# Optimization experiments

Measured on AMD Instinct MI355X. Metric: run time of the kernel, lower is better.

Reference implementation:

```python
import jax, jax.numpy as jnp
import numpy as np

N_BASIS = 8
CUTOFF = 5.0
NORM_FACTOR = 16.0


def setup_inputs() -> dict:
    key = jax.random.key(0)
    ks = jax.random.split(key, 10)
    N, E, C = 20000, 320000, 32
    s = 1.0 / np.sqrt(C)
    return {
        "node0": jax.random.normal(ks[0], (N, C), jnp.float32),
        "node1": jax.random.normal(ks[1], (N, C, 3), jnp.float32),
        "node2": jax.random.normal(ks[2], (N, C, 3, 3), jnp.float32),
        "rij": jax.random.normal(ks[3], (E, 3), jnp.float32) * 1.5,
        "Wrad": jax.random.normal(ks[4], (11, N_BASIS, C), jnp.float32) * 0.3,
        "U": jax.random.normal(ks[5], (3, C, C), jnp.float32) * s,
        "V": jax.random.normal(ks[6], (8, C, C), jnp.float32) * s,
        "Wg": jax.random.normal(ks[7], (3, C, C), jnp.float32) * s,
        "idx_i": jax.random.randint(ks[8], (E,), 0, N),
        "idx_j": jax.random.randint(ks[9], (E,), 0, N),
    }


def reference(node0, node1, node2, rij, Wrad, U, V, Wg, idx_i, idx_j):
    N, C = node0.shape
    # radial basis (Gaussian RBF * cosine cutoff envelope)
    dist = jnp.sqrt(jnp.sum(rij * rij, -1) + 1e-12)           # [E]
    rhat = rij / dist[:, None]                                 # [E,3]
    centers = jnp.linspace(0.5, CUTOFF, N_BASIS, dtype=node0.dtype)
    fc = 0.5 * (jnp.cos(jnp.pi * jnp.clip(dist / CUTOFF, 0.0, 1.0)) + 1.0)
    rbf = jnp.exp(-4.0 * (dist[:, None] - centers) ** 2) * fc[:, None]  # [E,B]
    # per-coupling-path radial filters: 11 paths (in_way, r_way, out_way)
    w = jnp.einsum('eb,pbc->pec', rbf, Wrad)                   # [11,E,C]
    # gather neighbor (node_j) features per edge
    g0 = node0[idx_j]                                          # [E,C]
    g1 = node1[idx_j]                                          # [E,C,3]
    g2 = node2[idx_j]                                          # [E,C,3,3]
    m1 = rhat                                                  # [E,3]
    m2 = rhat[:, :, None] * rhat[:, None, :]                   # [E,3,3]
    # graph conv: contract node_j tensor with r-way moment, weighted by radial filter
    # paths: 0:(0,0,0) 1:(0,1,1) 2:(0,2,2) 3:(1,0,1) 4:(1,1,0) 5:(1,1,2)
    #        6:(1,2,1) 7:(2,0,2) 8:(2,1,1) 9:(2,2,0) 10:(2,2,2)
    msg0 = (g0 * w[0]
            + jnp.einsum('eca,ea->ec', g1, m1) * w[4]
            + jnp.einsum('ecab,eab->ec', g2, m2) * w[9])
    msg1 = (jnp.einsum('ec,ea->eca', g0 * w[1], m1)
            + g1 * w[3][:, :, None]
            + jnp.einsum('eca,eab->ecb', g1, m2) * w[6][:, :, None]
            + jnp.einsum('ecab,eb->eca', g2, m1) * w[8][:, :, None])
    msg2 = (jnp.einsum('ec,eab->ecab', g0 * w[2], m2)
            + jnp.einsum('eca,eb->ecab', g1 * w[5][:, :, None], m1)
            + g2 * w[7][:, :, None, None]
            + jnp.einsum('ecab,ebd->ecad', g2, m2) * w[10][:, :, None, None])
    # scatter_add aggregation into per-atom features, normalized
    a0 = jax.ops.segment_sum(msg0, idx_i, num_segments=N) / NORM_FACTOR
    a1 = jax.ops.segment_sum(msg1, idx_i, num_segments=N) / NORM_FACTOR
    a2 = jax.ops.segment_sum(msg2, idx_i, num_segments=N) / NORM_FACTOR
    # multi-body self-interaction (2-body linear U + 3-body products V)
    y0 = (jnp.einsum('nc,cd->nd', a0, U[0])
          + jnp.einsum('nc,cd->nd', a0 * a0, V[0])
          + jnp.einsum('nc,cd->nd', jnp.einsum('nca,nca->nc', a1, a1), V[3])
          + jnp.einsum('nc,cd->nd', jnp.einsum('ncab,ncab->nc', a2, a2), V[6]))
    y1 = (jnp.einsum('nca,cd->nda', a1, U[1])
          + jnp.einsum('nca,cd->nda', a0[:, :, None] * a1, V[1])
          + jnp.einsum('nca,cd->nda', jnp.einsum('nca,ncab->ncb', a1, a2), V[5]))
    y2 = (jnp.einsum('ncab,cd->ndab', a2, U[2])
          + jnp.einsum('ncab,cd->ndab', a0[:, :, None, None] * a2, V[2])
          + jnp.einsum('ncab,cd->ndab', a1[:, :, :, None] * a1[:, :, None, :], V[4])
          + jnp.einsum('ncab,cd->ndab', jnp.einsum('ncab,ncbd->ncad', a2, a2), V[7]))
    # gated nonlinearity (scalar channel gates tensor ways) + residual add
    new0 = node0 + jax.nn.silu(y0 @ Wg[0])
    new1 = node1 + y1 * jax.nn.silu(y0 @ Wg[1])[:, :, None]
    new2 = node2 + y2 * jax.nn.silu(y0 @ Wg[2])[:, :, None, None]
    return (new0, new1, new2)
```

## Files before the change

kernel.cpp:

```cpp
#include <hip/hip_runtime.h>
#include <hip/hip_fp16.h>

#define NCH 32
#define NB 8
#define NPB 8

typedef __attribute__((ext_vector_type(2))) _Float16 half2r;

__device__ __forceinline__ unsigned short f2h(float f) {
    return __half_as_ushort(__float2half_rn(f));
}
__device__ __forceinline__ float h2f_lo(unsigned int u) {
    half2r v = __builtin_bit_cast(half2r, u);
    return (float)v.x;
}
__device__ __forceinline__ float h2f_hi(unsigned int u) {
    half2r v = __builtin_bit_cast(half2r, u);
    return (float)v.y;
}
__device__ __forceinline__ unsigned int pack2h(float lo, float hi) {
    return (unsigned int)f2h(lo) | ((unsigned int)f2h(hi) << 16);
}

__device__ __forceinline__ float fdot2u(unsigned int a, unsigned int b, float c) {
#if __has_builtin(__builtin_amdgcn_fdot2)
    return __builtin_amdgcn_fdot2(__builtin_bit_cast(half2r, a),
                                  __builtin_bit_cast(half2r, b), c, false);
#else
    half2r av = __builtin_bit_cast(half2r, a);
    half2r bv = __builtin_bit_cast(half2r, b);
    return c + (float)av.x * (float)bv.x + (float)av.y * (float)bv.y;
#endif
}

__device__ __forceinline__ void acc8h(float& y, uint4 w, uint4 f) {
    y = fdot2u(w.x, f.x, y);
    y = fdot2u(w.y, f.y, y);
    y = fdot2u(w.z, f.z, y);
    y = fdot2u(w.w, f.w, y);
}
__device__ __forceinline__ void acc8fh(float& y, uint4 w, float4 a, float4 b) {
    y += h2f_lo(w.x) * a.x + h2f_hi(w.x) * a.y + h2f_lo(w.y) * a.z + h2f_hi(w.y) * a.w
       + h2f_lo(w.z) * b.x + h2f_hi(w.z) * b.y + h2f_lo(w.w) * b.z + h2f_hi(w.w) * b.w;
}

__global__ __launch_bounds__(256) void prep_kernel(
    const float* __restrict__ node0, const float* __restrict__ node1,
    const float* __restrict__ node2,
    const float* __restrict__ U, const float* __restrict__ V,
    const float* __restrict__ Wg, const float* __restrict__ Wrad,
    uint2* __restrict__ t0g, uint4* __restrict__ t1g,
    unsigned short* __restrict__ t2g,
    unsigned short* __restrict__ wswz, unsigned int* __restrict__ wradp,
    int N, int TB)
{
    __shared__ float s1[8 * 96];
    __shared__ float s2[8 * 288];
    const int bx = blockIdx.x;

    if (bx < TB) {
        const int nb0 = bx * 8;
        const int remN = N - nb0;
        if (remN >= 8) {
            const float4* src1 = reinterpret_cast<const float4*>(node1 + (size_t)nb0 * 96);
            float4* d1 = reinterpret_cast<float4*>(s1);
            for (int i = threadIdx.x; i < 192; i += 256) d1[i] = src1[i];
            const float4* src2 = reinterpret_cast<const float4*>(node2 + (size_t)nb0 * 288);
            float4* d2 = reinterpret_cast<float4*>(s2);
            for (int i = threadIdx.x; i < 576; i += 256) d2[i] = src2[i];
        } else {
            const int tot1 = remN * 96;
            for (int i = threadIdx.x; i < 768; i += 256)
                s1[i] = (i < tot1) ? node1[(size_t)nb0 * 96 + i] : 0.f;
            const int tot2 = remN * 288;
            for (int i = threadIdx.x; i < 2304; i += 256)
                s2[i] = (i < tot2) ? node2[(size_t)nb0 * 288 + i] : 0.f;
        }
        __syncthreads();

        const int g = threadIdx.x >> 5;
        const int c = threadIdx.x & 31;
        const int n = nb0 + g;
        if (n >= N) return;

        float G0 = node0[(size_t)n * 32 + c];
        float G1[3];
        #pragma unroll
        for (int a = 0; a < 3; ++a) G1[a] = s1[g * 96 + c * 3 + a];
        float G2[9];
        #pragma unroll
        for (int k = 0; k < 9; ++k) G2[k] = s2[g * 288 + c * 9 + k];

        const size_t b = ((size_t)n << 5) + c;
        uint2 P0;
        P0.x = pack2h(G0, G1[0]);
        P0.y = pack2h(G1[1], G1[2]);
        uint4 P1;
        P1.x = pack2h(G2[0], G2[1]);
        P1.y = pack2h(G2[2], G2[3]);
        P1.z = pack2h(G2[4], G2[5]);
        P1.w = pack2h(G2[6], G2[7]);
        t0g[b] = P0;
        t1g[b] = P1;
        t2g[b] = f2h(G2[8]);
        return;
    }

    const int r = bx - TB;
    if (r < 56) {
        int idx = r * 256 + threadIdx.x;
        if (idx >= 14 * 1024) return;
        int m = idx >> 10, rr = idx & 1023;
        int c = rr >> 5, d = rr & 31;
        float v;
        if (m < 3)       v = U[m * 1024 + c * 32 + d];
        else if (m < 11) v = V[(m - 3) * 1024 + c * 32 + d];
        else             v = Wg[(m - 11) * 1024 + c * 32 + d];
        wswz[m * 1024 + (c >> 3) * 256 + d * 8 + (c & 7)] = f2h(v);
        return;
    }

    {
        int idx = (r - 56) * 256 + threadIdx.x;
        if (idx >= 11 * 4 * 32) return;
        int c = idx & 31, bb = (idx >> 5) & 3, p = idx >> 7;
        float lo = Wrad[p * 256 + (2 * bb) * 32 + c] * (1.0f / 16.0f);
        float hi = Wrad[p * 256 + (2 * bb + 1) * 32 + c] * (1.0f / 16.0f);
        wradp[c * 44 + p * 4 + bb] = pack2h(lo, hi);
    }
}

__global__ __launch_bounds__(256) void hist_kernel(
    const int* __restrict__ idx_i, int* __restrict__ counts, int E)
{
    int e = blockIdx.x * 256 + threadIdx.x;
    if (e < E) atomicAdd(&counts[idx_i[e]], 1);
}

__global__ __launch_bounds__(256) void scan_reduce_kernel(
    const int* __restrict__ counts, int* __restrict__ blocksums, int N)
{
    const int tid = threadIdx.x;
    const int base = blockIdx.x * 1024;
    int v = 0;
    #pragma unroll
    for (int k = 0; k < 4; ++k) {
        int i = base + tid * 4 + k;
        if (i < N) v += counts[i];
    }
    #pragma unroll
    for (int off = 1; off < 64; off <<= 1) v += __shfl_xor(v, off, 64);
    __shared__ int wsum[4];
    if ((tid & 63) == 0) wsum[tid >> 6] = v;
    __syncthreads();
    if (tid == 0) blocksums[blockIdx.x] = wsum[0] + wsum[1] + wsum[2] + wsum[3];
}

__global__ void scan_top_kernel(
    const int* __restrict__ blocksums, int* __restrict__ bases,
    int* __restrict__ offsets, int nb, int N)
{
    int l = threadIdx.x;
    int v = (l < nb) ? blocksums[l] : 0;
    int incl = v;
    #pragma unroll
    for (int off = 1; off < 64; off <<= 1) {
        int t = __shfl_up(incl, off, 64);
        if (l >= off) incl += t;
    }
    if (l < nb) bases[l] = incl - v;
    if (l == nb - 1) offsets[N] = incl;
}

__global__ __launch_bounds__(256) void scan_write_kernel(
    int* __restrict__ cursor, const int* __restrict__ bases,
    int* __restrict__ offsets, int N)
{
    const int tid = threadIdx.x;
    const int i0 = blockIdx.x * 1024 + tid * 4;
    int v[4]; int lsum = 0;
    #pragma unroll
    for (int k = 0; k < 4; ++k) {
        int i = i0 + k;
        v[k] = (i < N) ? cursor[i] : 0;
        lsum += v[k];
    }
    int incl = lsum;
    #pragma unroll
    for (int off = 1; off < 64; off <<= 1) {
        int t = __shfl_up(incl, off, 64);
        if ((tid & 63) >= off) incl += t;
    }
    __shared__ int wsum[4];
    if ((tid & 63) == 63) wsum[tid >> 6] = incl;
    __syncthreads();
    int add = bases[blockIdx.x];
    for (int w = 0; w < (tid >> 6); ++w) add += wsum[w];
    int run = add + incl - lsum;
    #pragma unroll
    for (int k = 0; k < 4; ++k) {
        int i = i0 + k;
        if (i < N) { offsets[i] = run; cursor[i] = run; run += v[k]; }
    }
}

__global__ __launch_bounds__(256) void scatter_meta_kernel(
    const int* __restrict__ idx_i, const int* __restrict__ idx_j,
    const float* __restrict__ rij, int* __restrict__ cursor,
    int* __restrict__ jord, float4* __restrict__ meta2, int E)
{
    int e = blockIdx.x * 256 + threadIdx.x;
    if (e >= E) return;
    float rx = rij[3 * e + 0], ry = rij[3 * e + 1], rz = rij[3 * e + 2];
    float sq = rx * rx + ry * ry + rz * rz + 1e-12f;
    float inv = rsqrtf(sq);
    float dist = sq * inv;
    float tcl = fminf(dist * 0.2f, 1.0f);
    float fc = 0.5f * (__cosf(3.14159265358979f * tcl) + 1.0f);
    float rbf[NB];
    #pragma unroll
    for (int b = 0; b < NB; ++b) {
        float dd = dist - (0.5f + (float)b * (4.5f / 7.0f));
        rbf[b] = __expf(-4.0f * dd * dd) * fc;
    }
    unsigned int rb01 = pack2h(rbf[0], rbf[1]);
    unsigned int rb23 = pack2h(rbf[2], rbf[3]);
    unsigned int rb45 = pack2h(rbf[4], rbf[5]);
    unsigned int rb67 = pack2h(rbf[6], rbf[7]);
    int slot = atomicAdd(&cursor[idx_i[e]], 1);
    jord[slot] = idx_j[e];
    meta2[2 * slot + 0] = make_float4(rx * inv, ry * inv, rz * inv, __uint_as_float(rb01));
    meta2[2 * slot + 1] = make_float4(__uint_as_float(rb23), __uint_as_float(rb45),
                                      __uint_as_float(rb67), 0.0f);
}

__device__ __forceinline__ void edge_compute(
    uint2 P0, uint4 P1, unsigned short g28, float4 M0, float4 M1,
    const uint4 wrq[11], float& A0, float (&A1)[3], float (&A2)[9])
{
    const float h0 = M0.x, h1 = M0.y, h2 = M0.z;
    const unsigned int rb01 = __float_as_uint(M0.w);
    const unsigned int rb23 = __float_as_uint(M1.x);
    const unsigned int rb45 = __float_as_uint(M1.y);
    const unsigned int rb67 = __float_as_uint(M1.z);

    float w[11];
    #pragma unroll
    for (int p = 0; p < 11; ++p)
        w[p] = fdot2u(rb01, wrq[p].x,
               fdot2u(rb23, wrq[p].y,
               fdot2u(rb45, wrq[p].z,
               fdot2u(rb67, wrq[p].w, 0.0f))));

    const float G0 = h2f_lo(P0.x);
    float G1[3];
    G1[0] = h2f_hi(P0.x); G1[1] = h2f_lo(P0.y); G1[2] = h2f_hi(P0.y);
    float G2[9];
    G2[0] = h2f_lo(P1.x); G2[1] = h2f_hi(P1.x);
    G2[2] = h2f_lo(P1.y); G2[3] = h2f_hi(P1.y);
    G2[4] = h2f_lo(P1.z); G2[5] = h2f_hi(P1.z);
    G2[6] = h2f_lo(P1.w); G2[7] = h2f_hi(P1.w);
    G2[8] = __half2float(__ushort_as_half(g28));

    const float hh[3] = {h0, h1, h2};
    const float s1 = G1[0] * h0 + G1[1] * h1 + G1[2] * h2;
    float tt[3];
    #pragma unroll
    for (int a = 0; a < 3; ++a)
        tt[a] = G2[a * 3 + 0] * h0 + G2[a * 3 + 1] * h1 + G2[a * 3 + 2] * h2;
    const float s2 = tt[0] * h0 + tt[1] * h1 + tt[2] * h2;

    A0 += G0 * w[0] + s1 * w[4] + s2 * w[9];
    #pragma unroll
    for (int a = 0; a < 3; ++a)
        A1[a] += (G0 * w[1] + s1 * w[6]) * hh[a] + G1[a] * w[3] + tt[a] * w[8];
    #pragma unroll
    for (int a = 0; a < 3; ++a) {
        float pre = G0 * w[2] * hh[a] + G1[a] * w[5] + tt[a] * w[10];
        #pragma unroll
        for (int b = 0; b < 3; ++b)
            A2[a * 3 + b] += pre * hh[b] + G2[a * 3 + b] * w[7];
    }
}

__global__ __launch_bounds__(256) void aggregate_kernel(
    const uint2* __restrict__ t0g, const uint4* __restrict__ t1g,
    const unsigned short* __restrict__ t2g, const unsigned int* __restrict__ wradp,
    const int* __restrict__ jord, const float4* __restrict__ meta2,
    const int* __restrict__ offsets,
    float* __restrict__ a0, float* __restrict__ a1, float* __restrict__ a2,
    int N)
{
    const int lane = threadIdx.x & 63;
    const int c = lane & 31;
    const int side = lane >> 5;
    const int n = blockIdx.x * 4 + (threadIdx.x >> 6);
    if (n >= N) return;

    uint4 wrq[11];
    {
        const uint4* wrv = reinterpret_cast<const uint4*>(wradp) + c * 11;
        #pragma unroll
        for (int p = 0; p < 11; ++p) wrq[p] = wrv[p];
    }

    const int beg = offsets[n], end = offsets[n + 1];
    const int deg = end - beg;

    float A0 = 0.f;
    float A1[3] = {0.f, 0.f, 0.f};
    float A2[9] = {0.f, 0.f, 0.f, 0.f, 0.f, 0.f, 0.f, 0.f, 0.f};

    if (deg > 0) {
        const int last = end - 1;
        int eA = beg + side;
        int eB = eA + 2;
        int jA2 = jord[min(eA + 4, last)];
        int jB2 = jord[min(eB + 4, last)];

        uint2 P0A, P0B; uint4 P1A, P1B; unsigned short s2A, s2B;
        float4 M0A, M1A, M0B, M1B;
        {
            const int jA = jord[min(eA, last)];
            const size_t b = ((size_t)jA << 5) + c;
            P0A = t0g[b]; P1A = t1g[b]; s2A = t2g[b];
            const int em = min(eA, last);
            M0A = meta2[2 * em]; M1A = meta2[2 * em + 1];
        }
        {
            const int jB = jord[min(eB, last)];
            const size_t b = ((size_t)jB << 5) + c;
            P0B = t0g[b]; P1B = t1g[b]; s2B = t2g[b];
            const int em = min(eB, last);
            M0B = meta2[2 * em]; M1B = meta2[2 * em + 1];
        }

        const int M = (deg + 3) >> 2;

#define SLOT_STEP(P0s, P1s, s2s, M0s, M1s, eS, jS2)                         \
        {                                                                   \
            const uint2 P0 = P0s; const uint4 P1 = P1s;                     \
            const unsigned short g28 = s2s;                                 \
            const float4 Mm0 = M0s, Mm1 = M1s;                              \
            const bool v = (eS < end);                                      \
            const int eSn = eS + 4;                                         \
            {                                                               \
                const size_t b = ((size_t)jS2 << 5) + c;                    \
                P0s = t0g[b]; P1s = t1g[b]; s2s = t2g[b];                   \
                const int em = min(eSn, last);                              \
                M0s = meta2[2 * em]; M1s = meta2[2 * em + 1];               \
            }                                                               \
            jS2 = jord[min(eSn + 4, last)];                                 \
            if (v) edge_compute(P0, P1, g28, Mm0, Mm1, wrq, A0, A1, A2);    \
            eS = eSn;                                                       \
        }

        for (int m = 0; m < M; ++m) {
            SLOT_STEP(P0A, P1A, s2A, M0A, M1A, eA, jA2)
            SLOT_STEP(P0B, P1B, s2B, M0B, M1B, eB, jB2)
        }
#undef SLOT_STEP
    }

    A0 += __shfl_xor(A0, 32, 64);
    #pragma unroll
    for (int a = 0; a < 3; ++a) A1[a] += __shfl_xor(A1[a], 32, 64);
    #pragma unroll
    for (int k = 0; k < 9; ++k) A2[k] += __shfl_xor(A2[k], 32, 64);

    if (side == 0) {
        a0[n * 32 + c] = A0;
        #pragma unroll
        for (int a = 0; a < 3; ++a) a1[n * 96 + a * 32 + c] = A1[a];
        #pragma unroll
        for (int k = 0; k < 9; ++k) a2[n * 288 + k * 32 + c] = A2[k];
    }
}

__global__ __launch_bounds__(256) void node_kernel(
    const float* __restrict__ node0, const float* __restrict__ node1,
    const float* __restrict__ node2, const unsigned short* __restrict__ wswz,
    float* __restrict__ out0, float* __restrict__ out1, float* __restrict__ out2,
    int N)
{
    __shared__ alignas(16) unsigned short feat[NPB * 49 * 32];
    __shared__ alignas(16) float y0s[NPB][32];

    const uint4* __restrict__ W4 = reinterpret_cast<const uint4*>(wswz);

    const int g = threadIdx.x >> 5;
    const int lane = threadIdx.x & 31;
    const int n = blockIdx.x * NPB + g;
    const bool active = (n < N);

    if (active) {
        const int c = lane;
        float A0 = out0[n * 32 + c];
        float A1[3], A2[9];
        #pragma unroll
        for (int a = 0; a < 3; ++a) A1[a] = out1[n * 96 + a * 32 + c];
        #pragma unroll
        for (int k = 0; k < 9; ++k) A2[k] = out2[n * 288 + k * 32 + c];

        unsigned short* F = &feat[g * 49 * 32];
        F[0 * 32 + c] = f2h(A0);
        F[1 * 32 + c] = f2h(A0 * A0);
        F[2 * 32 + c] = f2h(A1[0] * A1[0] + A1[1] * A1[1] + A1[2] * A1[2]);
        float n2 = 0.f;
        #pragma unroll
        for (int k = 0; k < 9; ++k) n2 += A2[k] * A2[k];
        F[3 * 32 + c] = f2h(n2);
        #pragma unroll
        for (int a = 0; a < 3; ++a) {
            F[(4 + a) * 32 + c] = f2h(A1[a]);
            F[(7 + a) * 32 + c] = f2h(A0 * A1[a]);
        }
        #pragma unroll
        for (int b = 0; b < 3; ++b) {
            float s = A1[0] * A2[0 * 3 + b] + A1[1] * A2[1 * 3 + b] + A1[2] * A2[2 * 3 + b];
            F[(10 + b) * 32 + c] = f2h(s);
        }
        #pragma unroll
        for (int k = 0; k < 9; ++k) {
            F[(13 + k) * 32 + c] = f2h(A2[k]);
            F[(22 + k) * 32 + c] = f2h(A0 * A2[k]);
        }
        #pragma unroll
        for (int a = 0; a < 3; ++a)
            #pragma unroll
            for (int b = 0; b < 3; ++b)
                F[(31 + a * 3 + b) * 32 + c] = f2h(A1[a] * A1[b]);
        #pragma unroll
        for (int a = 0; a < 3; ++a)
            #pragma unroll
            for (int dd = 0; dd < 3; ++dd) {
                float s = A2[a * 3 + 0] * A2[0 * 3 + dd] + A2[a * 3 + 1] * A2[1 * 3 + dd]
                        + A2[a * 3 + 2] * A2[2 * 3 + dd];
                F[(40 + a * 3 + dd) * 32 + c] = f2h(s);
            }
    }
    __syncthreads();

    const int d = lane;
    float y0v = 0.f;
    float y1v[3] = {0.f, 0.f, 0.f};
    float y2v[9] = {0.f, 0.f, 0.f, 0.f, 0.f, 0.f, 0.f, 0.f, 0.f};

    if (active) {
        const uint4* F4 = reinterpret_cast<const uint4*>(&feat[g * 49 * 32]);
        for (int q = 0; q < 4; ++q) {
            const int q32d = q * 32 + d;
            acc8h(y0v, W4[0 * 128 + q32d], F4[0 * 4 + q]);
            acc8h(y0v, W4[3 * 128 + q32d], F4[1 * 4 + q]);
            acc8h(y0v, W4[6 * 128 + q32d], F4[2 * 4 + q]);
            acc8h(y0v, W4[9 * 128 + q32d], F4[3 * 4 + q]);
            uint4 wU1 = W4[1 * 128 + q32d];
            uint4 wV1 = W4[4 * 128 + q32d];
            uint4 wV5 = W4[8 * 128 + q32d];
            #pragma unroll
            for (int a = 0; a < 3; ++a) {
                acc8h(y1v[a], wU1, F4[(4 + a) * 4 + q]);
                acc8h(y1v[a], wV1, F4[(7 + a) * 4 + q]);
                acc8h(y1v[a], wV5, F4[(10 + a) * 4 + q]);
            }
            uint4 wU2 = W4[2 * 128 + q32d];
            uint4 wV2 = W4[5 * 128 + q32d];
            uint4 wV4 = W4[7 * 128 + q32d];
            uint4 wV7 = W4[10 * 128 + q32d];
            #pragma unroll
            for (int k = 0; k < 9; ++k) {
                acc8h(y2v[k], wU2, F4[(13 + k) * 4 + q]);
                acc8h(y2v[k], wV2, F4[(22 + k) * 4 + q]);
                acc8h(y2v[k], wV4, F4[(31 + k) * 4 + q]);
                acc8h(y2v[k], wV7, F4[(40 + k) * 4 + q]);
            }
        }
        y0s[g][d] = y0v;
    }
    __syncthreads();

    if (!active) return;

    float t0 = 0.f, t1 = 0.f, t2 = 0.f;
    {
        const float4* Y4 = reinterpret_cast<const float4*>(y0s[g]);
        #pragma unroll
        for (int q = 0; q < 4; ++q) {
            const int q32d = q * 32 + d;
            float4 ya = Y4[2 * q], yb = Y4[2 * q + 1];
            acc8fh(t0, W4[11 * 128 + q32d], ya, yb);
            acc8fh(t1, W4[12 * 128 + q32d], ya, yb);
            acc8fh(t2, W4[13 * 128 + q32d], ya, yb);
        }
    }
    float s0 = t0 / (1.0f + __expf(-t0));
    float s1 = t1 / (1.0f + __expf(-t1));
    float s2 = t2 / (1.0f + __expf(-t2));

    out0[n * 32 + d] = node0[n * 32 + d] + s0;
    #pragma unroll
    for (int a = 0; a < 3; ++a)
        out1[n * 96 + d * 3 + a] = node1[n * 96 + d * 3 + a] + y1v[a] * s1;
    #pragma unroll
    for (int k = 0; k < 9; ++k)
        out2[n * 288 + d * 9 + k] = node2[n * 288 + d * 9 + k] + y2v[k] * s2;
}

extern "C" void kernel_launch(void* const* d_in, const int* in_sizes, int n_in,
                              void* d_out, int out_size, void* d_ws, size_t ws_size,
                              hipStream_t stream)
{
    const float* node0 = (const float*)d_in[0];
    const float* node1 = (const float*)d_in[1];
    const float* node2 = (const float*)d_in[2];
    const float* rij   = (const float*)d_in[3];
    const float* Wrad  = (const float*)d_in[4];
    const float* U     = (const float*)d_in[5];
    const float* V     = (const float*)d_in[6];
    const float* Wg    = (const float*)d_in[7];
    const int* idx_i   = (const int*)d_in[8];
    const int* idx_j   = (const int*)d_in[9];

    const int N = in_sizes[0] / 32;
    const int E = in_sizes[3] / 3;

    float* out0 = (float*)d_out;
    float* out1 = out0 + (size_t)N * 32;
    float* out2 = out1 + (size_t)N * 96;

    size_t off = 0;
    auto walloc = [&](size_t bytes) -> void* {
        off = (off + 63) & ~(size_t)63;
        void* p = (char*)d_ws + off;
        off += bytes;
        return p;
    };
    int*    cursor    = (int*)   walloc((size_t)N * 4);
    int*    offsets   = (int*)   walloc((size_t)(N + 1) * 4);
    int*    blocksums = (int*)   walloc(64 * 4);
    int*    bases     = (int*)   walloc(64 * 4);
    int*    jord      = (int*)   walloc((size_t)E * 4);
    float4* meta2     = (float4*)walloc((size_t)E * 2 * sizeof(float4));
    uint2*  t0g       = (uint2*) walloc((size_t)N * 32 * sizeof(uint2));
    uint4*  t1g       = (uint4*) walloc((size_t)N * 32 * sizeof(uint4));
    unsigned short* t2g = (unsigned short*)walloc((size_t)N * 32 * 2);
    unsigned short* wswz = (unsigned short*)walloc(14 * 1024 * 2);
    unsigned int*  wradp = (unsigned int*)walloc(11 * 4 * 32 * 4);
    (void)ws_size;

    const int nb = (N + 1023) / 1024;
    const int TB = (N + 7) / 8;

    hipMemsetAsync(cursor, 0, (size_t)N * sizeof(int), stream);

    prep_kernel<<<dim3(TB + 56 + 6), dim3(256), 0, stream>>>(
        node0, node1, node2, U, V, Wg, Wrad, t0g, t1g, t2g, wswz, wradp, N, TB);
    hist_kernel<<<dim3((E + 255) / 256), dim3(256), 0, stream>>>(idx_i, cursor, E);
    scan_reduce_kernel<<<dim3(nb), dim3(256), 0, stream>>>(cursor, blocksums, N);
    scan_top_kernel<<<dim3(1), dim3(64), 0, stream>>>(blocksums, bases, offsets, nb, N);
    scan_write_kernel<<<dim3(nb), dim3(256), 0, stream>>>(cursor, bases, offsets, N);
    scatter_meta_kernel<<<dim3((E + 255) / 256), dim3(256), 0, stream>>>(
        idx_i, idx_j, rij, cursor, jord, meta2, E);

    aggregate_kernel<<<dim3((N + 3) / 4), dim3(256), 0, stream>>>(
        t0g, t1g, t2g, wradp, jord, meta2, offsets, out0, out1, out2, N);

    node_kernel<<<dim3((N + NPB - 1) / NPB), dim3(256), 0, stream>>>(
        node0, node1, node2, wswz, out0, out1, out2, N);
}
```

Baseline: 250.5 us.

## Pack edge metadata into fp16 with embedded neighbor index; fuse histogram into prep

```diff
diff --git a/kernel.cpp b/kernel.cpp
--- a/kernel.cpp
+++ b/kernel.cpp
@@ -49,10 +49,11 @@
     const float* __restrict__ node2,
     const float* __restrict__ U, const float* __restrict__ V,
     const float* __restrict__ Wg, const float* __restrict__ Wrad,
+    const int* __restrict__ idx_i, int* __restrict__ cursor,
     uint2* __restrict__ t0g, uint4* __restrict__ t1g,
     unsigned short* __restrict__ t2g,
     unsigned short* __restrict__ wswz, unsigned int* __restrict__ wradp,
-    int N, int TB)
+    int N, int E, int TB)
 {
     __shared__ float s1[8 * 96];
     __shared__ float s2[8 * 288];
@@ -119,22 +120,19 @@
         wswz[m * 1024 + (c >> 3) * 256 + d * 8 + (c & 7)] = f2h(v);
         return;
     }
-
-    {
+    if (r < 62) {
         int idx = (r - 56) * 256 + threadIdx.x;
         if (idx >= 11 * 4 * 32) return;
         int c = idx & 31, bb = (idx >> 5) & 3, p = idx >> 7;
         float lo = Wrad[p * 256 + (2 * bb) * 32 + c] * (1.0f / 16.0f);
         float hi = Wrad[p * 256 + (2 * bb + 1) * 32 + c] * (1.0f / 16.0f);
         wradp[c * 44 + p * 4 + bb] = pack2h(lo, hi);
-    }
-}
-
-__global__ __launch_bounds__(256) void hist_kernel(
-    const int* __restrict__ idx_i, int* __restrict__ counts, int E)
-{
-    int e = blockIdx.x * 256 + threadIdx.x;
-    if (e < E) atomicAdd(&counts[idx_i[e]], 1);
+        return;
+    }
+    {
+        int e = (r - 62) * 256 + threadIdx.x;
+        if (e < E) atomicAdd(&cursor[idx_i[e]], 1);
+    }
 }
 
 __global__ __launch_bounds__(256) void scan_reduce_kernel(
@@ -207,7 +205,7 @@
 __global__ __launch_bounds__(256) void scatter_meta_kernel(
     const int* __restrict__ idx_i, const int* __restrict__ idx_j,
     const float* __restrict__ rij, int* __restrict__ cursor,
-    int* __restrict__ jord, float4* __restrict__ meta2, int E)
+    uint2* __restrict__ mh, uint4* __restrict__ mr, int E)
 {
     int e = blockIdx.x * 256 + threadIdx.x;
     if (e >= E) return;
@@ -223,34 +221,28 @@
         float dd = dist - (0.5f + (float)b * (4.5f / 7.0f));
         rbf[b] = __expf(-4.0f * dd * dd) * fc;
     }
-    unsigned int rb01 = pack2h(rbf[0], rbf[1]);
-    unsigned int rb23 = pack2h(rbf[2], rbf[3]);
-    unsigned int rb45 = pack2h(rbf[4], rbf[5]);
-    unsigned int rb67 = pack2h(rbf[6], rbf[7]);
-    int slot = atomicAdd(&cursor[idx_i[e]], 1);
-    jord[slot] = idx_j[e];
-    meta2[2 * slot + 0] = make_float4(rx * inv, ry * inv, rz * inv, __uint_as_float(rb01));
-    meta2[2 * slot + 1] = make_float4(__uint_as_float(rb23), __uint_as_float(rb45),
-                                      __uint_as_float(rb67), 0.0f);
+    const int i = idx_i[e];
+    const unsigned int j = (unsigned int)idx_j[e];
+    int slot = atomicAdd(&cursor[i], 1);
+    mh[slot] = make_uint2(pack2h(rx * inv, ry * inv),
+                          (unsigned int)f2h(rz * inv) | (j << 16));
+    mr[slot] = make_uint4(pack2h(rbf[0], rbf[1]), pack2h(rbf[2], rbf[3]),
+                          pack2h(rbf[4], rbf[5]), pack2h(rbf[6], rbf[7]));
 }
 
 __device__ __forceinline__ void edge_compute(
-    uint2 P0, uint4 P1, unsigned short g28, float4 M0, float4 M1,
+    uint2 P0, uint4 P1, unsigned short g28, uint2 H, uint4 R,
     const uint4 wrq[11], float& A0, float (&A1)[3], float (&A2)[9])
 {
-    const float h0 = M0.x, h1 = M0.y, h2 = M0.z;
-    const unsigned int rb01 = __float_as_uint(M0.w);
-    const unsigned int rb23 = __float_as_uint(M1.x);
-    const unsigned int rb45 = __float_as_uint(M1.y);
-    const unsigned int rb67 = __float_as_uint(M1.z);
+    const float h0 = h2f_lo(H.x), h1 = h2f_hi(H.x), h2 = h2f_lo(H.y);
 
     float w[11];
     #pragma unroll
     for (int p = 0; p < 11; ++p)
-        w[p] = fdot2u(rb01, wrq[p].x,
-               fdot2u(rb23, wrq[p].y,
-               fdot2u(rb45, wrq[p].z,
-               fdot2u(rb67, wrq[p].w, 0.0f))));
+        w[p] = fdot2u(R.x, wrq[p].x,
+               fdot2u(R.y, wrq[p].y,
+               fdot2u(R.z, wrq[p].z,
+               fdot2u(R.w, wrq[p].w, 0.0f))));
 
     const float G0 = h2f_lo(P0.x);
     float G1[3];
@@ -286,7 +278,7 @@
 __global__ __launch_bounds__(256) void aggregate_kernel(
     const uint2* __restrict__ t0g, const uint4* __restrict__ t1g,
     const unsigned short* __restrict__ t2g, const unsigned int* __restrict__ wradp,
-    const int* __restrict__ jord, const float4* __restrict__ meta2,
+    const uint2* __restrict__ mh, const uint4* __restrict__ mr,
     const int* __restrict__ offsets,
     float* __restrict__ a0, float* __restrict__ a1, float* __restrict__ a2,
     int N)
@@ -315,49 +307,50 @@
         const int last = end - 1;
         int eA = beg + side;
         int eB = eA + 2;
-        int jA2 = jord[min(eA + 4, last)];
-        int jB2 = jord[min(eB + 4, last)];
-
+
+        uint2 HA, HB, MHA, MHB;
         uint2 P0A, P0B; uint4 P1A, P1B; unsigned short s2A, s2B;
-        float4 M0A, M1A, M0B, M1B;
+        uint4 RA, RB;
         {
-            const int jA = jord[min(eA, last)];
-            const size_t b = ((size_t)jA << 5) + c;
+            const int em = min(eA, last);
+            HA = mh[em];
+            const size_t b = ((size_t)(HA.y >> 16) << 5) + c;
             P0A = t0g[b]; P1A = t1g[b]; s2A = t2g[b];
-            const int em = min(eA, last);
-            M0A = meta2[2 * em]; M1A = meta2[2 * em + 1];
+            RA = mr[em];
+            MHA = mh[min(eA + 4, last)];
         }
         {
-            const int jB = jord[min(eB, last)];
-            const size_t b = ((size_t)jB << 5) + c;
+            const int em = min(eB, last);
+            HB = mh[em];
+            const size_t b = ((size_t)(HB.y >> 16) << 5) + c;
             P0B = t0g[b]; P1B = t1g[b]; s2B = t2g[b];
-            const int em = min(eB, last);
-            M0B = meta2[2 * em]; M1B = meta2[2 * em + 1];
+            RB = mr[em];
+            MHB = mh[min(eB + 4, last)];
         }
 
         const int M = (deg + 3) >> 2;
 
-#define SLOT_STEP(P0s, P1s, s2s, M0s, M1s, eS, jS2)                         \
+#define SLOT_STEP(P0s, P1s, s2s, Hs, Rs, MHs, eS)                           \
         {                                                                   \
             const uint2 P0 = P0s; const uint4 P1 = P1s;                     \
             const unsigned short g28 = s2s;                                 \
-            const float4 Mm0 = M0s, Mm1 = M1s;                              \
+            const uint2 Hc = Hs; const uint4 Rc = Rs;                       \
             const bool v = (eS < end);                                      \
             const int eSn = eS + 4;                                         \
             {                                                               \
-                const size_t b = ((size_t)jS2 << 5) + c;                    \
+                const size_t b = ((size_t)(MHs.y >> 16) << 5) + c;          \
                 P0s = t0g[b]; P1s = t1g[b]; s2s = t2g[b];                   \
-                const int em = min(eSn, last);                              \
-                M0s = meta2[2 * em]; M1s = meta2[2 * em + 1];               \
+                Rs = mr[min(eSn, last)];                                    \
             }                                                               \
-            jS2 = jord[min(eSn + 4, last)];                                 \
-            if (v) edge_compute(P0, P1, g28, Mm0, Mm1, wrq, A0, A1, A2);    \
+            Hs = MHs;                                                       \
+            MHs = mh[min(eSn + 4, last)];                                   \
+            if (v) edge_compute(P0, P1, g28, Hc, Rc, wrq, A0, A1, A2);      \
             eS = eSn;                                                       \
         }
 
         for (int m = 0; m < M; ++m) {
-            SLOT_STEP(P0A, P1A, s2A, M0A, M1A, eA, jA2)
-            SLOT_STEP(P0B, P1B, s2B, M0B, M1B, eB, jB2)
+            SLOT_STEP(P0A, P1A, s2A, HA, RA, MHA, eA)
+            SLOT_STEP(P0B, P1B, s2B, HB, RB, MHB, eB)
         }
 #undef SLOT_STEP
     }
@@ -539,8 +532,8 @@
     int*    offsets   = (int*)   walloc((size_t)(N + 1) * 4);
     int*    blocksums = (int*)   walloc(64 * 4);
     int*    bases     = (int*)   walloc(64 * 4);
-    int*    jord      = (int*)   walloc((size_t)E * 4);
-    float4* meta2     = (float4*)walloc((size_t)E * 2 * sizeof(float4));
+    uint2*  mh        = (uint2*) walloc((size_t)E * sizeof(uint2));
+    uint4*  mr        = (uint4*) walloc((size_t)E * sizeof(uint4));
     uint2*  t0g       = (uint2*) walloc((size_t)N * 32 * sizeof(uint2));
     uint4*  t1g       = (uint4*) walloc((size_t)N * 32 * sizeof(uint4));
     unsigned short* t2g = (unsigned short*)walloc((size_t)N * 32 * 2);
@@ -550,20 +543,21 @@
 
     const int nb = (N + 1023) / 1024;
     const int TB = (N + 7) / 8;
+    const int HB = (E + 255) / 256;
 
     hipMemsetAsync(cursor, 0, (size_t)N * sizeof(int), stream);
 
-    prep_kernel<<<dim3(TB + 56 + 6), dim3(256), 0, stream>>>(
-        node0, node1, node2, U, V, Wg, Wrad, t0g, t1g, t2g, wswz, wradp, N, TB);
-    hist_kernel<<<dim3((E + 255) / 256), dim3(256), 0, stream>>>(idx_i, cursor, E);
+    prep_kernel<<<dim3(TB + 62 + HB), dim3(256), 0, stream>>>(
+        node0, node1, node2, U, V, Wg, Wrad, idx_i, cursor,
+        t0g, t1g, t2g, wswz, wradp, N, E, TB);
     scan_reduce_kernel<<<dim3(nb), dim3(256), 0, stream>>>(cursor, blocksums, N);
     scan_top_kernel<<<dim3(1), dim3(64), 0, stream>>>(blocksums, bases, offsets, nb, N);
     scan_write_kernel<<<dim3(nb), dim3(256), 0, stream>>>(cursor, bases, offsets, N);
     scatter_meta_kernel<<<dim3((E + 255) / 256), dim3(256), 0, stream>>>(
-        idx_i, idx_j, rij, cursor, jord, meta2, E);
+        idx_i, idx_j, rij, cursor, mh, mr, E);
 
     aggregate_kernel<<<dim3((N + 3) / 4), dim3(256), 0, stream>>>(
-        t0g, t1g, t2g, wradp, jord, meta2, offsets, out0, out1, out2, N);
+        t0g, t1g, t2g, wradp, mh, mr, offsets, out0, out1, out2, N);
 
     node_kernel<<<dim3((N + NPB - 1) / NPB), dim3(256), 0, stream>>>(
         node0, node1, node2, wswz, out0, out1, out2, N);
```

New measurement: 249.1 us, median of 2. No clear change (-0.6%).
